# Kernel tuning notes

Hardware: AMD Instinct MI355X
Metric: run time of the kernel (lower is better)

Reference implementation:

```python
import jax, jax.numpy as jnp
import numpy as np
from functools import partial

# dims
BATCH, L, H = 1, 512, 2048
NH, HD = 64, 64            # num heads, head dim
INTER = NH * HD            # 4096
G, N = 4, 64               # n_groups, ssm state size
K = 4                      # conv kernel
CONV = INTER + 2 * G * N   # 4608
PROJ = INTER + CONV + NH   # z, xBC, dt
EPS = 1e-5


def rmsnorm(x, w, eps=EPS):
    xf = x.astype(jnp.float32)
    v = jnp.mean(xf * xf, axis=-1, keepdims=True)
    return (xf * jax.lax.rsqrt(v + eps)).astype(x.dtype) * w


def setup_inputs() -> dict:
    key = jax.random.key(0)
    ks = jax.random.split(key, 12)
    rn = lambda k, s, sc=1.0: sc * jax.random.normal(k, s, dtype=jnp.float32)
    return {
        "hidden_states": rn(ks[0], (BATCH, L, H)),
        "residual": rn(ks[1], (BATCH, L, H)),
        "norm_w": 1.0 + rn(ks[2], (H,), 0.02),
        "in_proj_w": rn(ks[3], (H, PROJ), 0.02),
        "conv_w": rn(ks[4], (CONV, K), 0.2),
        "conv_b": rn(ks[5], (CONV,), 0.02),
        "A_log": jnp.log(jax.random.uniform(ks[6], (NH,), minval=1.0, maxval=16.0)),
        "dt_bias": rn(ks[7], (NH,), 0.5),
        "D": rn(ks[8], (NH,), 0.5),
        "gn_w": 1.0 + rn(ks[9], (INTER,), 0.02),
        "out_proj_w": rn(ks[10], (INTER, H), 0.02),
    }


def reference(hidden_states, residual, norm_w, in_proj_w, conv_w, conv_b,
              A_log, dt_bias, D, gn_w, out_proj_w):
    B_ = hidden_states.shape[0]
    # fused add + RMSNorm (residual is not None path)
    x = hidden_states + residual
    new_residual = x
    hs = rmsnorm(x, norm_w)

    # in_proj: [B,L,H] -> [B,L,PROJ] split into z | xBC | dt
    proj = jnp.einsum('blh,hp->blp', hs, in_proj_w)
    z = proj[..., :INTER]
    xBC = proj[..., INTER:INTER + CONV]
    dt = proj[..., INTER + CONV:]

    # causal depthwise conv of width K, then SiLU
    xp = jnp.pad(xBC, ((0, 0), (K - 1, 0), (0, 0)))
    conv = sum(xp[:, k:k + L, :] * conv_w[None, None, :, k] for k in range(K))
    xBC = jax.nn.silu(conv + conv_b)

    xh = xBC[..., :INTER].reshape(B_, L, NH, HD)
    Bm = xBC[..., INTER:INTER + G * N].reshape(B_, L, G, N)
    Cm = xBC[..., INTER + G * N:].reshape(B_, L, G, N)

    dt = jax.nn.softplus(dt + dt_bias)          # [B,L,NH]
    A = -jnp.exp(A_log)                         # [NH]
    dA = jnp.exp(dt * A)                        # [B,L,NH]

    hpg = NH // G
    Bh = jnp.repeat(Bm, hpg, axis=2)            # [B,L,NH,N]
    Ch = jnp.repeat(Cm, hpg, axis=2)

    def step(h, inp):
        dA_t, dt_t, x_t, B_t, C_t = inp
        # h: [B,NH,HD,N]
        h = h * dA_t[:, :, None, None] + (dt_t[:, :, None] * x_t)[..., None] * B_t[:, :, None, :]
        y = jnp.einsum('bhdn,bhn->bhd', h, C_t)
        return h, y

    h0 = jnp.zeros((B_, NH, HD, N), dtype=jnp.float32)
    xs = (jnp.moveaxis(dA, 1, 0), jnp.moveaxis(dt, 1, 0), jnp.moveaxis(xh, 1, 0),
          jnp.moveaxis(Bh, 1, 0), jnp.moveaxis(Ch, 1, 0))
    _, ys = jax.lax.scan(step, h0, xs)          # [L,B,NH,HD]
    y = jnp.moveaxis(ys, 0, 1) + xh * D[None, None, :, None]
    y = y.reshape(B_, L, INTER)

    # gated RMSNorm then out_proj
    y = rmsnorm(y * jax.nn.silu(z), gn_w)
    out = jnp.einsum('bli,ih->blh', y, out_proj_w)
    return out, new_residual
```

## Files before the change

### kernel.cpp

```cpp
#include <hip/hip_runtime.h>
#include <stdint.h>

#define LSEQ 512
#define HDIM 2048
#define NH 64
#define HD 64
#define INTER 4096
#define NG 4
#define NSTATE 64
#define CONVC 4608
#define PROJC 8768
#define EPS 1e-5f
#define CL 64
#define NC 8
#define NHDN (NH * HD * NSTATE)

typedef __attribute__((ext_vector_type(8))) short bf16x8;
typedef __attribute__((ext_vector_type(4))) short short4v;
typedef __attribute__((ext_vector_type(4))) float f32x4;

__device__ __forceinline__ short f2bf(float f) {
  union { float f; uint32_t u; } v; v.f = f;
  uint32_t r = v.u + 0x7FFFu + ((v.u >> 16) & 1u);
  return (short)(r >> 16);
}

__device__ __forceinline__ uint32_t cvt_pk_bf16(float lo, float hi) {
  uint32_t r;
  asm("v_cvt_pk_bf16_f32 %0, %1, %2" : "=v"(r) : "v"(lo), "v"(hi));
  return r;
}

__device__ __forceinline__ float bf2f(short s) {
  union { uint32_t u; float f; } v; v.u = ((uint32_t)(uint16_t)s) << 16;
  return v.f;
}

__device__ __forceinline__ float siluf(float v) {
  return v / (1.f + expf(-v));
}

__device__ __forceinline__ int xcd_swizzle(int orig, int nwg) {
  int q = nwg >> 3, r = nwg & 7;
  int xcd = orig & 7, idx = orig >> 3;
  return (xcd < r ? xcd * (q + 1) : r * (q + 1) + (xcd - r) * q) + idx;
}

__global__ __launch_bounds__(256) void k_add_rmsnorm(
    const float* __restrict__ hid, const float* __restrict__ res,
    const float* __restrict__ w, float* __restrict__ resid_out,
    short* __restrict__ hsb) {
  __shared__ float sred[4];
  const int row = blockIdx.x, tid = threadIdx.x;
  const float4* h4 = (const float4*)(hid + (size_t)row * HDIM);
  const float4* r4 = (const float4*)(res + (size_t)row * HDIM);
  float4* ro4 = (float4*)(resid_out + (size_t)row * HDIM);
  float4 a0 = h4[tid], b0 = r4[tid];
  float4 a1 = h4[tid + 256], b1 = r4[tid + 256];
  float4 xa, xb;
  xa.x = a0.x + b0.x; xa.y = a0.y + b0.y; xa.z = a0.z + b0.z; xa.w = a0.w + b0.w;
  xb.x = a1.x + b1.x; xb.y = a1.y + b1.y; xb.z = a1.z + b1.z; xb.w = a1.w + b1.w;
  ro4[tid] = xa; ro4[tid + 256] = xb;
  float ss = xa.x*xa.x + xa.y*xa.y + xa.z*xa.z + xa.w*xa.w
           + xb.x*xb.x + xb.y*xb.y + xb.z*xb.z + xb.w*xb.w;
  #pragma unroll
  for (int off = 32; off >= 1; off >>= 1) ss += __shfl_down(ss, off);
  if ((tid & 63) == 0) sred[tid >> 6] = ss;
  __syncthreads();
  float tot = sred[0] + sred[1] + sred[2] + sred[3];
  float rs = rsqrtf(tot / (float)HDIM + EPS);
  int e0 = tid * 4, e1 = (tid + 256) * 4;
  short4v s0, s1;
  s0.x = f2bf(xa.x * rs * w[e0+0]); s0.y = f2bf(xa.y * rs * w[e0+1]);
  s0.z = f2bf(xa.z * rs * w[e0+2]); s0.w = f2bf(xa.w * rs * w[e0+3]);
  s1.x = f2bf(xb.x * rs * w[e1+0]); s1.y = f2bf(xb.y * rs * w[e1+1]);
  s1.z = f2bf(xb.z * rs * w[e1+2]); s1.w = f2bf(xb.w * rs * w[e1+3]);
  *(short4v*)(hsb + (size_t)row * HDIM + e0) = s0;
  *(short4v*)(hsb + (size_t)row * HDIM + e1) = s1;
}

__global__ __launch_bounds__(256) void k_transpose_cvt(
    const float* __restrict__ src, short* __restrict__ dst, int R, int C) {
  __shared__ float tile[32][33];
  const int tx = threadIdx.x & 31, ty = threadIdx.x >> 5;
  const int c0 = blockIdx.x * 32, r0 = blockIdx.y * 32;
  #pragma unroll
  for (int i = 0; i < 4; ++i)
    tile[ty + i*8][tx] = src[(size_t)(r0 + ty + i*8) * C + c0 + tx];
  __syncthreads();
  #pragma unroll
  for (int i = 0; i < 4; ++i)
    dst[(size_t)(c0 + ty + i*8) * R + r0 + tx] = f2bf(tile[tx][ty + i*8]);
}

template <int BM, int KS>
__global__ __launch_bounds__(256) void k_gemm_fB(
    const short* __restrict__ A, const float* __restrict__ Bw,
    float* __restrict__ C, int M, int N, int K) {
  __shared__ short lA[2][BM * 64];
  __shared__ short lB[2][64 * 64];
  const int tid = threadIdx.x, lane = tid & 63, wid = tid >> 6;
  constexpr int MR = BM / 32;
  constexpr int WROWS = BM / 2;

  const int NMB = M / BM, NNB = N / 64;
  const int nwg = NMB * NNB * KS;
  int wg = xcd_swizzle(blockIdx.x, nwg);
  const int mi = wg % NMB;
  int rest = wg / NMB;
  const int zi = (KS > 1) ? (rest % KS) : 0;
  const int ni = (KS > 1) ? (rest / KS) : rest;
  const int m0 = mi * BM, n0 = ni * 64;
  const int wm = wid >> 1, wn = wid & 1;

  const int lrow8 = lane >> 3;
  const int cswz = ((lane & 7) ^ lrow8) * 8;

  const int Kc = K / KS, kbase = zi * Kc;
  float* Cp = C + (size_t)zi * M * N;

  auto stageA = [&](int buf, int kt) {
    #pragma unroll
    for (int r2 = 0; r2 < MR; ++r2) {
      int idx = r2 * 4 + wid;
      __builtin_amdgcn_global_load_lds(
          (const __attribute__((address_space(1))) int*)(A + (size_t)(m0 + idx * 8 + lrow8) * K + kt + cswz),
          (__attribute__((address_space(3))) int*)(&lA[buf][idx * 512]),
          16, 0, 0);
    }
  };

  float breg[16];
  auto loadB = [&](int kt) {
    #pragma unroll
    for (int r = 0; r < 2; ++r)
      #pragma unroll
      for (int j = 0; j < 8; ++j)
        breg[r * 8 + j] = Bw[(size_t)(kt + wid * 16 + r * 8 + j) * N + n0 + lane];
  };
  auto writeB = [&](int buf) {
    #pragma unroll
    for (int r = 0; r < 2; ++r) {
      uint4 v;
      v.x = cvt_pk_bf16(breg[r*8+0], breg[r*8+1]);
      v.y = cvt_pk_bf16(breg[r*8+2], breg[r*8+3]);
      v.z = cvt_pk_bf16(breg[r*8+4], breg[r*8+5]);
      v.w = cvt_pk_bf16(breg[r*8+6], breg[r*8+7]);
      int ko = wid * 2 + r;
      *(uint4*)&lB[buf][lane * 64 + ((ko ^ (lane & 7)) << 3)] = v;
    }
  };

  f32x4 acc[MR][2] = {};
  const int lrow = lane & 15, lkb = (lane >> 4) * 8;
  const int NT = Kc >> 6;
  loadB(kbase);
  stageA(0, kbase);
  writeB(0);
  asm volatile("s_waitcnt vmcnt(0)" ::: "memory");
  __builtin_amdgcn_s_barrier();
  for (int t = 0; t < NT; ++t) {
    int cur = t & 1;
    if (t + 1 < NT) {
      loadB(kbase + (t + 1) * 64);
      stageA(cur ^ 1, kbase + (t + 1) * 64);
    }
    #pragma unroll
    for (int kk = 0; kk < 2; ++kk) {
      bf16x8 a[MR], b[2];
      #pragma unroll
      for (int m = 0; m < MR; ++m) {
        int row = wm * WROWS + m * 16 + lrow;
        int colel = (kk * 32 + lkb) ^ ((row & 7) << 3);
        a[m] = *(const bf16x8*)&lA[cur][row * 64 + colel];
      }
      #pragma unroll
      for (int n = 0; n < 2; ++n) {
        int row = wn * 32 + n * 16 + lrow;
        int colel = (kk * 32 + lkb) ^ ((row & 7) << 3);
        b[n] = *(const bf16x8*)&lB[cur][row * 64 + colel];
      }
      #pragma unroll
      for (int m = 0; m < MR; ++m)
        #pragma unroll
        for (int n = 0; n < 2; ++n)
          acc[m][n] = __builtin_amdgcn_mfma_f32_16x16x32_bf16(a[m], b[n], acc[m][n], 0, 0, 0);
    }
    if (t + 1 < NT) writeB(cur ^ 1);
    asm volatile("s_waitcnt vmcnt(0)" ::: "memory");
    __builtin_amdgcn_s_barrier();
  }
  #pragma unroll
  for (int m = 0; m < MR; ++m) {
    int row = m0 + wm * WROWS + m * 16 + (lane >> 4) * 4;
    int col = n0 + wn * 32 + (lane & 15);
    #pragma unroll
    for (int n = 0; n < 2; ++n)
      #pragma unroll
      for (int r = 0; r < 4; ++r)
        Cp[(size_t)(row + r) * N + col + n * 16] = acc[m][n][r];
  }
}

template <int BM, int KS>
__global__ __launch_bounds__(256) void k_gemm_bf16(
    const short* __restrict__ A, const short* __restrict__ B,
    float* __restrict__ C, int M, int N, int K) {
  __shared__ short lA[2][BM * 64];
  __shared__ short lB[2][64 * 64];
  const int tid = threadIdx.x;
  const int lane = tid & 63, wid = tid >> 6;
  constexpr int MR = BM / 32;
  constexpr int WROWS = BM / 2;

  const int NMB = M / BM, NNB = N / 64;
  const int nwg = NMB * NNB * KS;
  int wg = xcd_swizzle(blockIdx.x, nwg);
  const int mi = wg % NMB;
  int rest = wg / NMB;
  const int zi = (KS > 1) ? (rest % KS) : 0;
  const int ni = (KS > 1) ? (rest / KS) : rest;
  const int m0 = mi * BM, n0 = ni * 64;
  const int wm = wid >> 1, wn = wid & 1;

  const int lrow8 = lane >> 3;
  const int cswz = ((lane & 7) ^ lrow8) * 8;

  const int Kc = K / KS;
  const int kbase = zi * Kc;
  float* Cp = C + (size_t)zi * M * N;

  auto stage = [&](int buf, int kt) {
    #pragma unroll
    for (int r2 = 0; r2 < MR; ++r2) {
      int idx = r2 * 4 + wid;
      __builtin_amdgcn_global_load_lds(
          (const __attribute__((address_space(1))) int*)(A + (size_t)(m0 + idx * 8 + lrow8) * K + kt + cswz),
          (__attribute__((address_space(3))) int*)(&lA[buf][idx * 512]),
          16, 0, 0);
    }
    #pragma unroll
    for (int r2 = 0; r2 < 2; ++r2) {
      int idx = r2 * 4 + wid;
      __builtin_amdgcn_global_load_lds(
          (const __attribute__((address_space(1))) int*)(B + (size_t)(n0 + idx * 8 + lrow8) * K + kt + cswz),
          (__attribute__((address_space(3))) int*)(&lB[buf][idx * 512]),
          16, 0, 0);
    }
  };

  f32x4 acc[MR][2] = {};
  const int lrow = lane & 15, lkb = (lane >> 4) * 8;
  const int NT = Kc >> 6;
  stage(0, kbase);
  for (int t = 0; t < NT; ++t) {
    int cur = t & 1;
    if (t + 1 < NT) {
      stage(cur ^ 1, kbase + (t + 1) * 64);
      if constexpr (MR == 2) asm volatile("s_waitcnt vmcnt(4)" ::: "memory");
      else                   asm volatile("s_waitcnt vmcnt(6)" ::: "memory");
    } else {
      asm volatile("s_waitcnt vmcnt(0)" ::: "memory");
    }
    __builtin_amdgcn_s_barrier();
    #pragma unroll
    for (int kk = 0; kk < 2; ++kk) {
      bf16x8 a[MR], b[2];
      #pragma unroll
      for (int m = 0; m < MR; ++m) {
        int row = wm * WROWS + m * 16 + lrow;
        int colel = (kk * 32 + lkb) ^ ((row & 7) << 3);
        a[m] = *(const bf16x8*)&lA[cur][row * 64 + colel];
      }
      #pragma unroll
      for (int n = 0; n < 2; ++n) {
        int row = wn * 32 + n * 16 + lrow;
        int colel = (kk * 32 + lkb) ^ ((row & 7) << 3);
        b[n] = *(const bf16x8*)&lB[cur][row * 64 + colel];
      }
      #pragma unroll
      for (int m = 0; m < MR; ++m)
        #pragma unroll
        for (int n = 0; n < 2; ++n)
          acc[m][n] = __builtin_amdgcn_mfma_f32_16x16x32_bf16(a[m], b[n], acc[m][n], 0, 0, 0);
    }
    __builtin_amdgcn_s_barrier();
  }
  #pragma unroll
  for (int m = 0; m < MR; ++m) {
    int row = m0 + wm * WROWS + m * 16 + (lane >> 4) * 4;
    int col = n0 + wn * 32 + (lane & 15);
    #pragma unroll
    for (int n = 0; n < 2; ++n)
      #pragma unroll
      for (int r = 0; r < 4; ++r)
        Cp[(size_t)(row + r) * N + col + n * 16] = acc[m][n][r];
  }
}

__global__ __launch_bounds__(256) void k_reduce2(
    const float* __restrict__ p, float* __restrict__ out, int n) {
  int i = (blockIdx.x * 256 + threadIdx.x) * 4;
  float4 a = *(const float4*)(p + i);
  float4 b = *(const float4*)(p + n + i);
  float4 o;
  o.x = a.x + b.x; o.y = a.y + b.y; o.z = a.z + b.z; o.w = a.w + b.w;
  *(float4*)(out + i) = o;
}

__global__ __launch_bounds__(256) void k_conv(
    const float* __restrict__ proj, const float* __restrict__ cw,
    const float* __restrict__ cb, const float* __restrict__ A_log,
    const float* __restrict__ dt_bias, float* __restrict__ convo,
    float* __restrict__ dtb, float* __restrict__ ldab) {
  const int l0 = blockIdx.y * 64;
  if (blockIdx.x == CONVC / 256) {
    #pragma unroll
    for (int i = 0; i < 16; ++i) {
      int idx = threadIdx.x + i * 256;
      int l = l0 + (idx >> 6), h = idx & 63;
      float v = proj[(size_t)l * PROJC + INTER + CONVC + h] + dt_bias[h];
      float dt = v > 20.f ? v : log1pf(expf(v));
      float lda = dt * (-expf(A_log[h]));
      dtb[h * LSEQ + l] = dt;
      ldab[h * LSEQ + l] = lda;
    }
    return;
  }
  const int c = blockIdx.x * 256 + threadIdx.x;
  const float w0 = cw[c*4+0], w1 = cw[c*4+1], w2 = cw[c*4+2], w3 = cw[c*4+3];
  const float bias = cb[c];
  float x0 = 0.f, x1 = 0.f, x2 = 0.f;
  if (l0 > 0) {
    x0 = proj[(size_t)(l0-3) * PROJC + INTER + c];
    x1 = proj[(size_t)(l0-2) * PROJC + INTER + c];
    x2 = proj[(size_t)(l0-1) * PROJC + INTER + c];
  }
  for (int l = l0; l < l0 + 64; ++l) {
    float x3 = proj[(size_t)l * PROJC + INTER + c];
    float accv = bias + x0*w0 + x1*w1 + x2*w2 + x3*w3;
    convo[(size_t)l * CONVC + c] = siluf(accv);
    x0 = x1; x1 = x2; x2 = x3;
  }
}

__global__ __launch_bounds__(256) void k_ssd(
    const float* __restrict__ convo, const float* __restrict__ dtb,
    const float* __restrict__ ldab, const float* __restrict__ Dp,
    float* __restrict__ ybuf, float* __restrict__ hend,
    float* __restrict__ Pbuf, float* __restrict__ cdbuf) {
  __shared__ __align__(16) short Xt[64 * 72];
  __shared__ __align__(16) short Bs[64 * 72];
  __shared__ __align__(16) short Cs[64 * 72];
  __shared__ __align__(16) short Btw[64 * 72];
  __shared__ __align__(16) short Ms[64 * 72];
  __shared__ float s_s[64], s_dt[64], s_w[64];
  const int c = blockIdx.x, head = blockIdx.y;
  const int g = head >> 4;
  const int tid = threadIdx.x, lane = tid & 63, wid = tid >> 6;
  const int l0 = c * CL;
  const float* xbase = convo + (size_t)l0 * CONVC + head * HD;
  const float* Bbase = convo + (size_t)l0 * CONVC + INTER + g * NSTATE;
  const float* Cbase = convo + (size_t)l0 * CONVC + INTER + NG * NSTATE + g * NSTATE;

  if (tid < 64) {
    float ps = ldab[head * LSEQ + l0 + tid];
    #pragma unroll
    for (int o = 1; o < 64; o <<= 1) {
      float u = __shfl_up(ps, o);
      if (tid >= o) ps += u;
    }
    float dtv = dtb[head * LSEQ + l0 + tid];
    s_s[tid] = ps;
    s_dt[tid] = dtv;
    float s63 = __shfl(ps, 63);
    s_w[tid] = __expf(s63 - ps) * dtv;
    cdbuf[head * LSEQ + l0 + tid] = __expf(ps);
    if (tid == 63) Pbuf[c * NH + head] = __expf(ps);
  }
  #pragma unroll
  for (int rep = 0; rep < 4; ++rep) {
    int l = (tid >> 4) + rep * 16;
    int d = (tid & 15) * 4;
    size_t roff = (size_t)l * CONVC;
    float4 xv = *(const float4*)(xbase + roff + d);
    Xt[(d + 0) * 72 + l] = f2bf(xv.x);
    Xt[(d + 1) * 72 + l] = f2bf(xv.y);
    Xt[(d + 2) * 72 + l] = f2bf(xv.z);
    Xt[(d + 3) * 72 + l] = f2bf(xv.w);
    float4 bv = *(const float4*)(Bbase + roff + d);
    uint2 bu; bu.x = cvt_pk_bf16(bv.x, bv.y); bu.y = cvt_pk_bf16(bv.z, bv.w);
    *(uint2*)&Bs[l * 72 + d] = bu;
    float4 cv = *(const float4*)(Cbase + roff + d);
    uint2 cu; cu.x = cvt_pk_bf16(cv.x, cv.y); cu.y = cvt_pk_bf16(cv.z, cv.w);
    *(uint2*)&Cs[l * 72 + d] = cu;
  }
  __syncthreads();
  #pragma unroll
  for (int rep = 0; rep < 16; ++rep) {
    int idx = rep * 256 + tid;
    int l = idx >> 6, n = idx & 63;
    Btw[n * 72 + l] = f2bf(bf2f(Bs[l * 72 + n]) * s_w[l]);
  }
  __syncthreads();
  const int lrow = lane & 15, lkb = (lane >> 4) * 8;
  f32x4 sacc[4] = {};
  f32x4 hacc[4] = {};
  #pragma unroll
  for (int kk = 0; kk < 2; ++kk) {
    bf16x8 ac = *(const bf16x8*)&Cs[(wid * 16 + lrow) * 72 + kk * 32 + lkb];
    bf16x8 ax = *(const bf16x8*)&Xt[(wid * 16 + lrow) * 72 + kk * 32 + lkb];
    #pragma unroll
    for (int t4 = 0; t4 < 4; ++t4) {
      bf16x8 bb = *(const bf16x8*)&Bs[(t4 * 16 + lrow) * 72 + kk * 32 + lkb];
      bf16x8 bw = *(const bf16x8*)&Btw[(t4 * 16 + lrow) * 72 + kk * 32 + lkb];
      sacc[t4] = __builtin_amdgcn_mfma_f32_16x16x32_bf16(ac, bb, sacc[t4], 0, 0, 0);
      hacc[t4] = __builtin_amdgcn_mfma_f32_16x16x32_bf16(ax, bw, hacc[t4], 0, 0, 0);
    }
  }
  float* hb = hend + ((size_t)c * NH + head) * (HD * NSTATE);
  #pragma unroll
  for (int t4 = 0; t4 < 4; ++t4) {
    int j = t4 * 16 + lrow;
    float sj = s_s[j], dtj = s_dt[j];
    #pragma unroll
    for (int r = 0; r < 4; ++r) {
      int i = wid * 16 + (lane >> 4) * 4 + r;
      float m = (j <= i) ? __expf(s_s[i] - sj) * dtj * sacc[t4][r] : 0.f;
      Ms[i * 72 + j] = f2bf(m);
      hb[i * NSTATE + j] = hacc[t4][r];
    }
  }
  __syncthreads();
  f32x4 yacc[4] = {};
  #pragma unroll
  for (int kk = 0; kk < 2; ++kk) {
    bf16x8 am = *(const bf16x8*)&Ms[(wid * 16 + lrow) * 72 + kk * 32 + lkb];
    #pragma unroll
    for (int t4 = 0; t4 < 4; ++t4) {
      bf16x8 bx = *(const bf16x8*)&Xt[(t4 * 16 + lrow) * 72 + kk * 32 + lkb];
      yacc[t4] = __builtin_amdgcn_mfma_f32_16x16x32_bf16(am, bx, yacc[t4], 0, 0, 0);
    }
  }
  const float Dv = Dp[head];
  #pragma unroll
  for (int t4 = 0; t4 < 4; ++t4) {
    int d = t4 * 16 + lrow;
    #pragma unroll
    for (int r = 0; r < 4; ++r) {
      int i = wid * 16 + (lane >> 4) * 4 + r;
      float xv = bf2f(Xt[d * 72 + i]);
      ybuf[(size_t)(l0 + i) * INTER + head * HD + d] = yacc[t4][r] + xv * Dv;
    }
  }
}

__global__ __launch_bounds__(256) void k_scan_combine(
    const float* __restrict__ hend, const float* __restrict__ Pbuf,
    float* __restrict__ hinbuf) {
  const int e = blockIdx.x * 256 + threadIdx.x;
  const int head = e >> 12;
  float h = 0.f;
  #pragma unroll
  for (int c = 1; c < NC; ++c) {
    h = Pbuf[(c - 1) * NH + head] * h + hend[(size_t)(c - 1) * NHDN + e];
    hinbuf[(size_t)c * NHDN + e] = h;
  }
}

__global__ __launch_bounds__(256) void k_scan_fixup(
    const float* __restrict__ convo, const float* __restrict__ hinbuf,
    const float* __restrict__ cdbuf, float* __restrict__ ybuf) {
  __shared__ float sh[NSTATE][HD + 1];
  __shared__ float sc[CL][NSTATE];
  __shared__ float scd[CL];
  const int bid = blockIdx.x;
  const int c = (bid >> 6) + 1, head = bid & 63, g = head >> 4;
  const int t = threadIdx.x;
  #pragma unroll
  for (int i = 0; i < 16; ++i) {
    int idx = t + i * 256;
    int d = idx >> 6, n = idx & 63;
    sh[n][d] = hinbuf[(size_t)c * NHDN + head * (HD * NSTATE) + idx];
  }
  #pragma unroll
  for (int i = 0; i < 16; ++i) {
    int idx = t + i * 256;
    int ll = idx >> 6, n = idx & 63;
    sc[ll][n] = convo[(size_t)(c * CL + ll) * CONVC + INTER + NG * NSTATE + g * NSTATE + n];
  }
  if (t < CL) scd[t] = cdbuf[head * LSEQ + c * CL + t];
  __syncthreads();
  const int d = t & 63, w = t >> 6;
  #pragma unroll
  for (int i = 0; i < 4; ++i) {
    int l0 = i * 16 + w * 4;
    float a0 = 0.f, a1 = 0.f, a2 = 0.f, a3 = 0.f;
    for (int n = 0; n < NSTATE; ++n) {
      float hv = sh[n][d];
      a0 += hv * sc[l0 + 0][n];
      a1 += hv * sc[l0 + 1][n];
      a2 += hv * sc[l0 + 2][n];
      a3 += hv * sc[l0 + 3][n];
    }
    size_t base = (size_t)(c * CL + l0) * INTER + head * HD + d;
    ybuf[base + 0 * INTER] += scd[l0 + 0] * a0;
    ybuf[base + 1 * INTER] += scd[l0 + 1] * a1;
    ybuf[base + 2 * INTER] += scd[l0 + 2] * a2;
    ybuf[base + 3 * INTER] += scd[l0 + 3] * a3;
  }
}

__global__ __launch_bounds__(256) void k_gated_norm(
    const float* __restrict__ ybuf, const float* __restrict__ proj,
    const float* __restrict__ gw, short* __restrict__ y2b) {
  __shared__ float sred[4];
  const int row = blockIdx.x, tid = threadIdx.x;
  const float4* y4 = (const float4*)(ybuf + (size_t)row * INTER);
  const float4* z4 = (const float4*)(proj + (size_t)row * PROJC);
  float g[16];
  float ss = 0.f;
  #pragma unroll
  for (int i = 0; i < 4; ++i) {
    float4 y = y4[tid + i * 256];
    float4 z = z4[tid + i * 256];
    float g0 = y.x * siluf(z.x), g1 = y.y * siluf(z.y);
    float g2 = y.z * siluf(z.z), g3 = y.w * siluf(z.w);
    g[i*4+0] = g0; g[i*4+1] = g1; g[i*4+2] = g2; g[i*4+3] = g3;
    ss += g0*g0 + g1*g1 + g2*g2 + g3*g3;
  }
  #pragma unroll
  for (int off = 32; off >= 1; off >>= 1) ss += __shfl_down(ss, off);
  if ((tid & 63) == 0) sred[tid >> 6] = ss;
  __syncthreads();
  float tot = sred[0] + sred[1] + sred[2] + sred[3];
  float rs = rsqrtf(tot / (float)INTER + EPS);
  #pragma unroll
  for (int i = 0; i < 4; ++i) {
    int e = (tid + i * 256) * 4;
    short4v s;
    s.x = f2bf(g[i*4+0] * rs * gw[e+0]);
    s.y = f2bf(g[i*4+1] * rs * gw[e+1]);
    s.z = f2bf(g[i*4+2] * rs * gw[e+2]);
    s.w = f2bf(g[i*4+3] * rs * gw[e+3]);
    *(short4v*)(y2b + (size_t)row * INTER + e) = s;
  }
}

extern "C" void kernel_launch(void* const* d_in, const int* in_sizes, int n_in,
                              void* d_out, int out_size, void* d_ws, size_t ws_size,
                              hipStream_t stream) {
  const float* hid     = (const float*)d_in[0];
  const float* res     = (const float*)d_in[1];
  const float* norm_w  = (const float*)d_in[2];
  const float* w1      = (const float*)d_in[3];
  const float* cw      = (const float*)d_in[4];
  const float* cb      = (const float*)d_in[5];
  const float* A_log   = (const float*)d_in[6];
  const float* dt_bias = (const float*)d_in[7];
  const float* Dp      = (const float*)d_in[8];
  const float* gw      = (const float*)d_in[9];
  const float* w2      = (const float*)d_in[10];

  float* out = (float*)d_out;
  float* resid_out = out + (size_t)LSEQ * HDIM;

  char* ws = (char*)d_ws;
  short* hsb  = (short*)(ws);
  float* hend   = (float*)(ws + 2097152);
  float* p2     = (float*)(ws + 2097152);
  float* hinbuf = (float*)(ws + 10485760);
  float* Pbuf   = (float*)(ws + 18874368);
  float* cdbuf  = (float*)(ws + 18876416);
  float* proj = (float*)(ws + 38010880);
  float* convo= (float*)(ws + 55967744);
  float* dtb  = (float*)(ws + 65404928);
  float* ldab = (float*)(ws + 65536000);
  float* ybuf = (float*)(ws + 65667072);
  short* y2b  = (short*)(ws + 74055680);
  short* w2t  = (short*)(ws + 78249984);

  k_add_rmsnorm<<<LSEQ, 256, 0, stream>>>(hid, res, norm_w, resid_out, hsb);
  k_gemm_fB<128, 1><<<(LSEQ/128)*(PROJC/64), 256, 0, stream>>>(hsb, w1, proj, LSEQ, PROJC, HDIM);
  k_conv<<<dim3(CONVC/256 + 1, NC), 256, 0, stream>>>(proj, cw, cb, A_log, dt_bias, convo, dtb, ldab);
  k_ssd<<<dim3(NC, NH), 256, 0, stream>>>(convo, dtb, ldab, Dp, ybuf, hend, Pbuf, cdbuf);
  k_scan_combine<<<NHDN/256, 256, 0, stream>>>(hend, Pbuf, hinbuf);
  k_scan_fixup<<<(NC-1)*NH, 256, 0, stream>>>(convo, hinbuf, cdbuf, ybuf);
  k_gated_norm<<<LSEQ, 256, 0, stream>>>(ybuf, proj, gw, y2b);
  k_transpose_cvt<<<dim3(HDIM/32, INTER/32), 256, 0, stream>>>(w2, w2t, INTER, HDIM);
  k_gemm_bf16<64, 2><<<(LSEQ/64)*(HDIM/64)*2, 256, 0, stream>>>(y2b, w2t, p2, LSEQ, HDIM, INTER);
  k_reduce2<<<LSEQ*HDIM/1024, 256, 0, stream>>>(p2, out, LSEQ*HDIM);
}
```

Baseline: 142.2 us.

## Store in_proj outputs and conv output as bf16 in split buffers

The first GEMM now writes its output into three separate buffers: z and xBC as bf16, and dt as fp32. The conv kernel reads bf16 xBC and writes its SiLU output as bf16. The SSD, fixup and gated-norm kernels then read bf16 directly instead of fp32 that they previously converted. This roughly halves the intermediate traffic through memory, at the cost of rounding z and the conv input/output to bf16 earlier, which may shift accuracy.

Measured after the change: 135.9 us. 4.4% less time.

```diff
diff --git a/kernel.cpp b/kernel.cpp
--- a/kernel.cpp
+++ b/kernel.cpp
@@ -93,31 +93,26 @@
     dst[(size_t)(c0 + ty + i*8) * R + r0 + tx] = f2bf(tile[tx][ty + i*8]);
 }
 
-template <int BM, int KS>
-__global__ __launch_bounds__(256) void k_gemm_fB(
+__global__ __launch_bounds__(256) void k_gemm1(
     const short* __restrict__ A, const float* __restrict__ Bw,
-    float* __restrict__ C, int M, int N, int K) {
+    short* __restrict__ zbf, short* __restrict__ xbc,
+    float* __restrict__ dtf) {
+  constexpr int BM = 128, MR = 4, WROWS = 64;
+  const int M = LSEQ, N = PROJC, K = HDIM;
   __shared__ short lA[2][BM * 64];
   __shared__ short lB[2][64 * 64];
   const int tid = threadIdx.x, lane = tid & 63, wid = tid >> 6;
-  constexpr int MR = BM / 32;
-  constexpr int WROWS = BM / 2;
 
   const int NMB = M / BM, NNB = N / 64;
-  const int nwg = NMB * NNB * KS;
+  const int nwg = NMB * NNB;
   int wg = xcd_swizzle(blockIdx.x, nwg);
   const int mi = wg % NMB;
-  int rest = wg / NMB;
-  const int zi = (KS > 1) ? (rest % KS) : 0;
-  const int ni = (KS > 1) ? (rest / KS) : rest;
+  const int ni = wg / NMB;
   const int m0 = mi * BM, n0 = ni * 64;
   const int wm = wid >> 1, wn = wid & 1;
 
   const int lrow8 = lane >> 3;
   const int cswz = ((lane & 7) ^ lrow8) * 8;
-
-  const int Kc = K / KS, kbase = zi * Kc;
-  float* Cp = C + (size_t)zi * M * N;
 
   auto stageA = [&](int buf, int kt) {
     #pragma unroll
@@ -153,17 +148,17 @@
 
   f32x4 acc[MR][2] = {};
   const int lrow = lane & 15, lkb = (lane >> 4) * 8;
-  const int NT = Kc >> 6;
-  loadB(kbase);
-  stageA(0, kbase);
+  const int NT = K >> 6;
+  loadB(0);
+  stageA(0, 0);
   writeB(0);
   asm volatile("s_waitcnt vmcnt(0)" ::: "memory");
   __builtin_amdgcn_s_barrier();
   for (int t = 0; t < NT; ++t) {
     int cur = t & 1;
     if (t + 1 < NT) {
-      loadB(kbase + (t + 1) * 64);
-      stageA(cur ^ 1, kbase + (t + 1) * 64);
+      loadB((t + 1) * 64);
+      stageA(cur ^ 1, (t + 1) * 64);
     }
     #pragma unroll
     for (int kk = 0; kk < 2; ++kk) {
@@ -193,12 +188,20 @@
   #pragma unroll
   for (int m = 0; m < MR; ++m) {
     int row = m0 + wm * WROWS + m * 16 + (lane >> 4) * 4;
-    int col = n0 + wn * 32 + (lane & 15);
-    #pragma unroll
-    for (int n = 0; n < 2; ++n)
-      #pragma unroll
-      for (int r = 0; r < 4; ++r)
-        Cp[(size_t)(row + r) * N + col + n * 16] = acc[m][n][r];
+    #pragma unroll
+    for (int n = 0; n < 2; ++n) {
+      int coll = wn * 32 + n * 16 + (lane & 15);
+      #pragma unroll
+      for (int r = 0; r < 4; ++r) {
+        float v = acc[m][n][r];
+        if (ni < 64)
+          zbf[(size_t)(row + r) * INTER + n0 + coll] = f2bf(v);
+        else if (ni < 136)
+          xbc[(size_t)(row + r) * CONVC + (n0 - INTER) + coll] = f2bf(v);
+        else
+          dtf[(row + r) * 64 + coll] = v;
+      }
+    }
   }
 }
 
@@ -309,17 +312,18 @@
 }
 
 __global__ __launch_bounds__(256) void k_conv(
-    const float* __restrict__ proj, const float* __restrict__ cw,
-    const float* __restrict__ cb, const float* __restrict__ A_log,
-    const float* __restrict__ dt_bias, float* __restrict__ convo,
-    float* __restrict__ dtb, float* __restrict__ ldab) {
+    const short* __restrict__ xbc, const float* __restrict__ dtf,
+    const float* __restrict__ cw, const float* __restrict__ cb,
+    const float* __restrict__ A_log, const float* __restrict__ dt_bias,
+    short* __restrict__ convo, float* __restrict__ dtb,
+    float* __restrict__ ldab) {
   const int l0 = blockIdx.y * 64;
   if (blockIdx.x == CONVC / 256) {
     #pragma unroll
     for (int i = 0; i < 16; ++i) {
       int idx = threadIdx.x + i * 256;
       int l = l0 + (idx >> 6), h = idx & 63;
-      float v = proj[(size_t)l * PROJC + INTER + CONVC + h] + dt_bias[h];
+      float v = dtf[l * 64 + h] + dt_bias[h];
       float dt = v > 20.f ? v : log1pf(expf(v));
       float lda = dt * (-expf(A_log[h]));
       dtb[h * LSEQ + l] = dt;
@@ -332,20 +336,20 @@
   const float bias = cb[c];
   float x0 = 0.f, x1 = 0.f, x2 = 0.f;
   if (l0 > 0) {
-    x0 = proj[(size_t)(l0-3) * PROJC + INTER + c];
-    x1 = proj[(size_t)(l0-2) * PROJC + INTER + c];
-    x2 = proj[(size_t)(l0-1) * PROJC + INTER + c];
+    x0 = bf2f(xbc[(size_t)(l0-3) * CONVC + c]);
+    x1 = bf2f(xbc[(size_t)(l0-2) * CONVC + c]);
+    x2 = bf2f(xbc[(size_t)(l0-1) * CONVC + c]);
   }
   for (int l = l0; l < l0 + 64; ++l) {
-    float x3 = proj[(size_t)l * PROJC + INTER + c];
+    float x3 = bf2f(xbc[(size_t)l * CONVC + c]);
     float accv = bias + x0*w0 + x1*w1 + x2*w2 + x3*w3;
-    convo[(size_t)l * CONVC + c] = siluf(accv);
+    convo[(size_t)l * CONVC + c] = f2bf(siluf(accv));
     x0 = x1; x1 = x2; x2 = x3;
   }
 }
 
 __global__ __launch_bounds__(256) void k_ssd(
-    const float* __restrict__ convo, const float* __restrict__ dtb,
+    const short* __restrict__ convo, const float* __restrict__ dtb,
     const float* __restrict__ ldab, const float* __restrict__ Dp,
     float* __restrict__ ybuf, float* __restrict__ hend,
     float* __restrict__ Pbuf, float* __restrict__ cdbuf) {
@@ -359,9 +363,9 @@
   const int g = head >> 4;
   const int tid = threadIdx.x, lane = tid & 63, wid = tid >> 6;
   const int l0 = c * CL;
-  const float* xbase = convo + (size_t)l0 * CONVC + head * HD;
-  const float* Bbase = convo + (size_t)l0 * CONVC + INTER + g * NSTATE;
-  const float* Cbase = convo + (size_t)l0 * CONVC + INTER + NG * NSTATE + g * NSTATE;
+  const short* xbase = convo + (size_t)l0 * CONVC + head * HD;
+  const short* Bbase = convo + (size_t)l0 * CONVC + INTER + g * NSTATE;
+  const short* Cbase = convo + (size_t)l0 * CONVC + INTER + NG * NSTATE + g * NSTATE;
 
   if (tid < 64) {
     float ps = ldab[head * LSEQ + l0 + tid];
@@ -383,17 +387,13 @@
     int l = (tid >> 4) + rep * 16;
     int d = (tid & 15) * 4;
     size_t roff = (size_t)l * CONVC;
-    float4 xv = *(const float4*)(xbase + roff + d);
-    Xt[(d + 0) * 72 + l] = f2bf(xv.x);
-    Xt[(d + 1) * 72 + l] = f2bf(xv.y);
-    Xt[(d + 2) * 72 + l] = f2bf(xv.z);
-    Xt[(d + 3) * 72 + l] = f2bf(xv.w);
-    float4 bv = *(const float4*)(Bbase + roff + d);
-    uint2 bu; bu.x = cvt_pk_bf16(bv.x, bv.y); bu.y = cvt_pk_bf16(bv.z, bv.w);
-    *(uint2*)&Bs[l * 72 + d] = bu;
-    float4 cv = *(const float4*)(Cbase + roff + d);
-    uint2 cu; cu.x = cvt_pk_bf16(cv.x, cv.y); cu.y = cvt_pk_bf16(cv.z, cv.w);
-    *(uint2*)&Cs[l * 72 + d] = cu;
+    short4v xv = *(const short4v*)(xbase + roff + d);
+    Xt[(d + 0) * 72 + l] = xv.x;
+    Xt[(d + 1) * 72 + l] = xv.y;
+    Xt[(d + 2) * 72 + l] = xv.z;
+    Xt[(d + 3) * 72 + l] = xv.w;
+    *(short4v*)&Bs[l * 72 + d] = *(const short4v*)(Bbase + roff + d);
+    *(short4v*)&Cs[l * 72 + d] = *(const short4v*)(Cbase + roff + d);
   }
   __syncthreads();
   #pragma unroll
@@ -469,7 +469,7 @@
 }
 
 __global__ __launch_bounds__(256) void k_scan_fixup(
-    const float* __restrict__ convo, const float* __restrict__ hinbuf,
+    const short* __restrict__ convo, const float* __restrict__ hinbuf,
     const float* __restrict__ cdbuf, float* __restrict__ ybuf) {
   __shared__ float sh[NSTATE][HD + 1];
   __shared__ float sc[CL][NSTATE];
@@ -487,7 +487,7 @@
   for (int i = 0; i < 16; ++i) {
     int idx = t + i * 256;
     int ll = idx >> 6, n = idx & 63;
-    sc[ll][n] = convo[(size_t)(c * CL + ll) * CONVC + INTER + NG * NSTATE + g * NSTATE + n];
+    sc[ll][n] = bf2f(convo[(size_t)(c * CL + ll) * CONVC + INTER + NG * NSTATE + g * NSTATE + n]);
   }
   if (t < CL) scd[t] = cdbuf[head * LSEQ + c * CL + t];
   __syncthreads();
@@ -512,20 +512,20 @@
 }
 
 __global__ __launch_bounds__(256) void k_gated_norm(
-    const float* __restrict__ ybuf, const float* __restrict__ proj,
+    const float* __restrict__ ybuf, const short* __restrict__ zbf,
     const float* __restrict__ gw, short* __restrict__ y2b) {
   __shared__ float sred[4];
   const int row = blockIdx.x, tid = threadIdx.x;
   const float4* y4 = (const float4*)(ybuf + (size_t)row * INTER);
-  const float4* z4 = (const float4*)(proj + (size_t)row * PROJC);
+  const short4v* z4 = (const short4v*)(zbf + (size_t)row * INTER);
   float g[16];
   float ss = 0.f;
   #pragma unroll
   for (int i = 0; i < 4; ++i) {
     float4 y = y4[tid + i * 256];
-    float4 z = z4[tid + i * 256];
-    float g0 = y.x * siluf(z.x), g1 = y.y * siluf(z.y);
-    float g2 = y.z * siluf(z.z), g3 = y.w * siluf(z.w);
+    short4v z = z4[tid + i * 256];
+    float g0 = y.x * siluf(bf2f(z.x)), g1 = y.y * siluf(bf2f(z.y));
+    float g2 = y.z * siluf(bf2f(z.z)), g3 = y.w * siluf(bf2f(z.w));
     g[i*4+0] = g0; g[i*4+1] = g1; g[i*4+2] = g2; g[i*4+3] = g3;
     ss += g0*g0 + g1*g1 + g2*g2 + g3*g3;
   }
@@ -572,8 +572,10 @@
   float* hinbuf = (float*)(ws + 10485760);
   float* Pbuf   = (float*)(ws + 18874368);
   float* cdbuf  = (float*)(ws + 18876416);
-  float* proj = (float*)(ws + 38010880);
-  float* convo= (float*)(ws + 55967744);
+  short* zbf  = (short*)(ws + 38010880);
+  short* xbc  = (short*)(ws + 42205184);
+  float* dtf  = (float*)(ws + 46923776);
+  short* convo= (short*)(ws + 55967744);
   float* dtb  = (float*)(ws + 65404928);
   float* ldab = (float*)(ws + 65536000);
   float* ybuf = (float*)(ws + 65667072);
@@ -581,12 +583,12 @@
   short* w2t  = (short*)(ws + 78249984);
 
   k_add_rmsnorm<<<LSEQ, 256, 0, stream>>>(hid, res, norm_w, resid_out, hsb);
-  k_gemm_fB<128, 1><<<(LSEQ/128)*(PROJC/64), 256, 0, stream>>>(hsb, w1, proj, LSEQ, PROJC, HDIM);
-  k_conv<<<dim3(CONVC/256 + 1, NC), 256, 0, stream>>>(proj, cw, cb, A_log, dt_bias, convo, dtb, ldab);
+  k_gemm1<<<(LSEQ/128)*(PROJC/64), 256, 0, stream>>>(hsb, w1, zbf, xbc, dtf);
+  k_conv<<<dim3(CONVC/256 + 1, NC), 256, 0, stream>>>(xbc, dtf, cw, cb, A_log, dt_bias, convo, dtb, ldab);
   k_ssd<<<dim3(NC, NH), 256, 0, stream>>>(convo, dtb, ldab, Dp, ybuf, hend, Pbuf, cdbuf);
   k_scan_combine<<<NHDN/256, 256, 0, stream>>>(hend, Pbuf, hinbuf);
   k_scan_fixup<<<(NC-1)*NH, 256, 0, stream>>>(convo, hinbuf, cdbuf, ybuf);
-  k_gated_norm<<<LSEQ, 256, 0, stream>>>(ybuf, proj, gw, y2b);
+  k_gated_norm<<<LSEQ, 256, 0, stream>>>(ybuf, zbf, gw, y2b);
   k_transpose_cvt<<<dim3(HDIM/32, INTER/32), 256, 0, stream>>>(w2, w2t, INTER, HDIM);
   k_gemm_bf16<64, 2><<<(LSEQ/64)*(HDIM/64)*2, 256, 0, stream>>>(y2b, w2t, p2, LSEQ, HDIM, INTER);
   k_reduce2<<<LSEQ*HDIM/1024, 256, 0, stream>>>(p2, out, LSEQ*HDIM);
```
